# Kernel optimization log

Measured on AMD Instinct MI355X. Metric: run time of the kernel, lower is better.

Reference implementation:

```python
import jax, jax.numpy as jnp
import numpy as np

N, F_IN, F_OUT, P, E = 50000, 64, 64, 8, 800000


def setup_inputs() -> dict:
    key = jax.random.key(0)
    ks = jax.random.split(key, 11)
    s = 0.05
    X = jax.random.normal(ks[0], (N, F_IN, P), jnp.float32)
    edge_index = jax.random.randint(ks[1], (2, E), 0, N)
    edge_weight = jax.random.uniform(ks[2], (E,), jnp.float32)
    # Stacked ChebConv (K=2) params for gates [i, f, c, o]
    Wx0 = jax.random.normal(ks[3], (4, F_IN, F_OUT), jnp.float32) * s
    Wx1 = jax.random.normal(ks[4], (4, F_IN, F_OUT), jnp.float32) * s
    bx = jax.random.normal(ks[5], (4, F_OUT), jnp.float32) * s
    Wh0 = jax.random.normal(ks[6], (4, F_OUT, F_OUT), jnp.float32) * s
    Wh1 = jax.random.normal(ks[7], (4, F_OUT, F_OUT), jnp.float32) * s
    bh = jax.random.normal(ks[8], (4, F_OUT), jnp.float32) * s
    wc = jax.random.normal(ks[9], (3, F_OUT), jnp.float32) * s  # peepholes for i, f, o
    bg = jax.random.normal(ks[10], (4, F_OUT), jnp.float32) * s  # gate biases i, f, c, o
    return dict(X=X, edge_index=edge_index, edge_weight=edge_weight,
                Wx0=Wx0, Wx1=Wx1, bx=bx, Wh0=Wh0, Wh1=Wh1, bh=bh, wc=wc, bg=bg)


def reference(X, edge_index, edge_weight, Wx0, Wx1, bx, Wh0, Wh1, bh, wc, bg):
    src, dst = edge_index[0], edge_index[1]
    # sym-normalized Laplacian, scaled by 2/lambda_max with lambda_max=2, minus I:
    # L_hat = -D^{-1/2} A D^{-1/2}  (diagonal cancels exactly in ChebConv.__norm__)
    deg = jax.ops.segment_sum(edge_weight, src, num_segments=N)
    dis = jnp.where(deg > 0, jax.lax.rsqrt(jnp.maximum(deg, 1e-12)), 0.0)
    wn = -dis[src] * edge_weight * dis[dst]  # [E]

    def cheb(x, W0, W1, b):
        # ChebConv K=2: T0(x)=x, T1(x)=L_hat x ; out = x@W0 + (L_hat x)@W1 + b
        tx1 = jax.ops.segment_sum(wn[:, None] * x[src], dst, num_segments=N)
        return x @ W0 + tx1 @ W1 + b

    def step(Xp):  # one GConvLSTM step from zero hidden/cell state (H=None, C=None)
        H = jnp.zeros((N, F_OUT), X.dtype)
        C = jnp.zeros((N, F_OUT), X.dtype)
        I = jax.nn.sigmoid(cheb(Xp, Wx0[0], Wx1[0], bx[0]) + cheb(H, Wh0[0], Wh1[0], bh[0]) + wc[0] * C + bg[0])
        Fg = jax.nn.sigmoid(cheb(Xp, Wx0[1], Wx1[1], bx[1]) + cheb(H, Wh0[1], Wh1[1], bh[1]) + wc[1] * C + bg[1])
        T = jnp.tanh(cheb(Xp, Wx0[2], Wx1[2], bx[2]) + cheb(H, Wh0[2], Wh1[2], bh[2]) + bg[2])
        Cn = Fg * C + I * T
        O = jax.nn.sigmoid(cheb(Xp, Wx0[3], Wx1[3], bx[3]) + cheb(H, Wh0[3], Wh1[3], bh[3]) + wc[2] * Cn + bg[3])
        return O * jnp.tanh(Cn)

    # periods are independent (fresh zero state each period) -> vmap then sum
    Hs = jax.vmap(step)(jnp.moveaxis(X, 2, 0))  # [P, N, F_OUT]
    return Hs.sum(axis=0)
```

## Files before the change

### kernel.cpp

```cpp
#include <hip/hip_runtime.h>
#include <hip/hip_fp16.h>

#define NN 50000
#define EE 800000
#define FF 64
#define PP 8
#define NPAD 50048
#define ELLW 64

typedef _Float16 half8 __attribute__((ext_vector_type(8)));
typedef _Float16 half4 __attribute__((ext_vector_type(4)));
typedef float floatx4 __attribute__((ext_vector_type(4)));

static constexpr size_t al512(size_t x) { return (x + 511) & ~size_t(511); }
static constexpr size_t OFF_DEG  = 0;
static constexpr size_t OFF_CNT  = al512(OFF_DEG  + (size_t)NN*4);
static constexpr size_t OFF_DIS  = al512(OFF_CNT  + (size_t)NN*4);
static constexpr size_t OFF_ELL  = al512(OFF_DIS  + (size_t)NN*4);
static constexpr size_t OFF_BIAS = al512(OFF_ELL  + (size_t)NN*ELLW*8);
static constexpr size_t OFF_WC2  = al512(OFF_BIAS + 192*4);
static constexpr size_t OFF_WFRG = al512(OFF_WC2  + 64*4);
static constexpr size_t OFF_XB   = al512(OFF_WFRG + (size_t)24576*2);
static constexpr size_t OFF_TB   = al512(OFF_XB   + (size_t)NPAD*512*2);

__global__ void k_build(const int* __restrict__ src, const int* __restrict__ dst,
                        const float* __restrict__ ew,
                        float* __restrict__ deg, int* __restrict__ cnt,
                        int2* __restrict__ ell) {
    int e = blockIdx.x * 256 + threadIdx.x;
    if (e < EE) {
        int s = src[e], d = dst[e];
        float w = ew[e];
        atomicAdd(deg + s, w);
        int pos = atomicAdd(cnt + d, 1);
        if (pos < ELLW) {
            int2 pr; pr.x = s; pr.y = __float_as_int(w);
            ell[(size_t)d * ELLW + pos] = pr;
        }
    }
}

__global__ void k_prep(const float* __restrict__ Wx0, const float* __restrict__ Wx1,
                       const float* __restrict__ bx, const float* __restrict__ bh,
                       const float* __restrict__ wc, const float* __restrict__ bg,
                       const float* __restrict__ deg,
                       _Float16* __restrict__ Wfrag, float* __restrict__ biasv,
                       float* __restrict__ wc2, float* __restrict__ dis) {
    int t = blockIdx.x * 256 + threadIdx.x;
    const int gmap[3] = {0, 2, 3};
    if (t < NN) {
        float dg = deg[t];
        dis[t] = dg > 0.f ? rsqrtf(fmaxf(dg, 1e-12f)) : 0.f;
    }
    if (t < 24576) {
        int j8 = t & 7;
        int lane = (t >> 3) & 63;
        int rem = t >> 9;
        int ct = rem % 12;
        int ks = rem / 12;
        int k = ks * 32 + (lane >> 4) * 8 + j8;
        int gp = ct >> 2;
        int g = gmap[gp];
        int j64 = (ct & 3) * 16 + (lane & 15);
        float val = (k < 64) ? Wx0[((size_t)g * 64 + k) * 64 + j64]
                             : Wx1[((size_t)g * 64 + (k - 64)) * 64 + j64];
        Wfrag[t] = (_Float16)val;
    }
    if (t < 192) {
        int gp = t / 64, j = t % 64;
        int g = gmap[gp];
        biasv[t] = bx[g * 64 + j] + bh[g * 64 + j] + bg[g * 64 + j];
    }
    if (t < 64) wc2[t] = wc[2 * 64 + t];
}

__global__ void k_xw(const float* __restrict__ X, _Float16* __restrict__ XB,
                     const float* __restrict__ dis, const int* __restrict__ cnt,
                     int2* __restrict__ ell) {
    __shared__ _Float16 tile[4][512];
    int wid = threadIdx.x >> 6, lane = threadIdx.x & 63;
    int n = blockIdx.x * 4 + wid;
    if (n >= NN) return;
    int cn = min(cnt[n], ELLW);
    if (lane < cn) {
        int2* p = ell + (size_t)n * ELLW + lane;
        int2 ed = *p;
        float w = dis[ed.x] * __int_as_float(ed.y);
        p->y = __float_as_int(w);
    }
    const float4* xp = (const float4*)(X + (size_t)n * 512 + lane * 8);
    float4 a = xp[0], b = xp[1];
    float v[8] = {a.x, a.y, a.z, a.w, b.x, b.y, b.z, b.w};
#pragma unroll
    for (int p = 0; p < PP; ++p)
        tile[wid][p * 64 + lane] = (_Float16)v[p];
    half8 vv = *(const half8*)&tile[wid][lane * 8];
    *(half8*)(XB + (size_t)n * 512 + lane * 8) = vv;
}

__global__ void k_spmm(const _Float16* __restrict__ XB, const int* __restrict__ cnt,
                       const float* __restrict__ dis, const int2* __restrict__ ell,
                       _Float16* __restrict__ TB, int n_base, int n_end) {
    int wid = threadIdx.x >> 6, lane = threadIdx.x & 63;
    int b = blockIdx.x;
    int half = b & 1;
    int n = n_base + (b >> 1) * 4 + wid;
    if (n >= n_end) return;
    float acc[4] = {0.f, 0.f, 0.f, 0.f};
    int cn = min(cnt[n], ELLW);
    float dn = dis[n];
    const int foff = half * 256 + lane * 4;
    if (cn > 0) {
        const int2* __restrict__ row = ell + (size_t)n * ELLW;
        int2 ed = row[min(lane, cn - 1)];
        int wli = (lane < cn) ? ed.y : 0;
        for (int base = 0; base < cn; base += 16) {
            half4 r[16];
            float wk[16];
#pragma unroll
            for (int u = 0; u < 16; ++u) {
                int srck = __builtin_amdgcn_readlane(ed.x, base + u);
                wk[u] = __int_as_float(__builtin_amdgcn_readlane(wli, base + u));
                r[u] = *(const half4*)(XB + (size_t)srck * 512 + foff);
            }
#pragma unroll
            for (int u = 0; u < 16; ++u) {
#pragma unroll
                for (int j = 0; j < 4; ++j) acc[j] += wk[u] * (float)r[u][j];
            }
        }
    }
    half4 st;
#pragma unroll
    for (int j = 0; j < 4; ++j) st[j] = (_Float16)(-dn * acc[j]);
    *(half4*)(TB + (size_t)n * 512 + foff) = st;
}

__device__ __forceinline__ float fast_rcp(float x) { return __builtin_amdgcn_rcpf(x); }
__device__ __forceinline__ float sigmoidf_fast(float x) {
    return fast_rcp(1.f + __expf(-x));
}
__device__ __forceinline__ float tanhf_fast(float x) {
    return 1.f - 2.f * fast_rcp(1.f + __expf(2.f * x));
}

__global__ __launch_bounds__(64) void k_gemm(const _Float16* __restrict__ XB,
                                             const _Float16* __restrict__ TB,
                                             const _Float16* __restrict__ Wfrag,
                                             const float* __restrict__ biasv,
                                             const float* __restrict__ wc2,
                                             float* __restrict__ out) {
    const int lane = threadIdx.x & 63;
    const half8* __restrict__ Wg8 = (const half8*)Wfrag;

    const int n0 = blockIdx.x * 32;
    const int jj = lane & 15, quad = lane >> 4;

    float bi[4], bc[4], bo[4], wcv[4];
#pragma unroll
    for (int c4 = 0; c4 < 4; ++c4) {
        int j = c4 * 16 + jj;
        bi[c4] = biasv[j];
        bc[c4] = biasv[64 + j];
        bo[c4] = biasv[128 + j];
        wcv[c4] = wc2[j];
    }

    const _Float16* __restrict__ x0 = XB + (size_t)(n0 + jj) * 512;
    const _Float16* __restrict__ x1 = XB + (size_t)(n0 + 16 + jj) * 512;
    const _Float16* __restrict__ t0 = TB + (size_t)(n0 + jj) * 512;
    const _Float16* __restrict__ t1 = TB + (size_t)(n0 + 16 + jj) * 512;

    floatx4 outacc[2][4];
#pragma unroll
    for (int r = 0; r < 2; ++r)
#pragma unroll
        for (int c4 = 0; c4 < 4; ++c4) outacc[r][c4] = (floatx4){0.f, 0.f, 0.f, 0.f};

#pragma unroll 1
    for (int p = 0; p < PP; ++p) {
        const int o = p * 64 + quad * 8;
        half8 a00 = *(const half8*)(x0 + o);
        half8 a01 = *(const half8*)(x0 + o + 32);
        half8 a02 = *(const half8*)(t0 + o);
        half8 a03 = *(const half8*)(t0 + o + 32);
        half8 a10 = *(const half8*)(x1 + o);
        half8 a11 = *(const half8*)(x1 + o + 32);
        half8 a12 = *(const half8*)(t1 + o);
        half8 a13 = *(const half8*)(t1 + o + 32);
#pragma unroll
        for (int c4 = 0; c4 < 4; ++c4) {
            floatx4 ai0 = {0.f,0.f,0.f,0.f}, ac0 = {0.f,0.f,0.f,0.f}, ao0 = {0.f,0.f,0.f,0.f};
            floatx4 ai1 = {0.f,0.f,0.f,0.f}, ac1 = {0.f,0.f,0.f,0.f}, ao1 = {0.f,0.f,0.f,0.f};
#pragma unroll
            for (int ks = 0; ks < 4; ++ks) {
                half8 bfi = Wg8[(ks * 12 + c4) * 64 + lane];
                half8 bfc = Wg8[(ks * 12 + 4 + c4) * 64 + lane];
                half8 bfo = Wg8[(ks * 12 + 8 + c4) * 64 + lane];
                half8 a0 = (ks == 0) ? a00 : (ks == 1) ? a01 : (ks == 2) ? a02 : a03;
                half8 a1 = (ks == 0) ? a10 : (ks == 1) ? a11 : (ks == 2) ? a12 : a13;
                ai0 = __builtin_amdgcn_mfma_f32_16x16x32_f16(a0, bfi, ai0, 0, 0, 0);
                ai1 = __builtin_amdgcn_mfma_f32_16x16x32_f16(a1, bfi, ai1, 0, 0, 0);
                ac0 = __builtin_amdgcn_mfma_f32_16x16x32_f16(a0, bfc, ac0, 0, 0, 0);
                ac1 = __builtin_amdgcn_mfma_f32_16x16x32_f16(a1, bfc, ac1, 0, 0, 0);
                ao0 = __builtin_amdgcn_mfma_f32_16x16x32_f16(a0, bfo, ao0, 0, 0, 0);
                ao1 = __builtin_amdgcn_mfma_f32_16x16x32_f16(a1, bfo, ao1, 0, 0, 0);
            }
#pragma unroll
            for (int rr = 0; rr < 4; ++rr) {
                float I0 = sigmoidf_fast(ai0[rr] + bi[c4]);
                float T0 = tanhf_fast(ac0[rr] + bc[c4]);
                float Cn0 = I0 * T0;
                float O0 = sigmoidf_fast(ao0[rr] + bo[c4] + wcv[c4] * Cn0);
                outacc[0][c4][rr] += O0 * tanhf_fast(Cn0);
                float I1 = sigmoidf_fast(ai1[rr] + bi[c4]);
                float T1 = tanhf_fast(ac1[rr] + bc[c4]);
                float Cn1 = I1 * T1;
                float O1 = sigmoidf_fast(ao1[rr] + bo[c4] + wcv[c4] * Cn1);
                outacc[1][c4][rr] += O1 * tanhf_fast(Cn1);
            }
        }
    }
#pragma unroll
    for (int r = 0; r < 2; ++r)
#pragma unroll
        for (int c4 = 0; c4 < 4; ++c4)
#pragma unroll
            for (int rr = 0; rr < 4; ++rr) {
                int n = n0 + r * 16 + quad * 4 + rr;
                if (n < NN) out[(size_t)n * 64 + c4 * 16 + jj] = outacc[r][c4][rr];
            }
}

extern "C" void kernel_launch(void* const* d_in, const int* in_sizes, int n_in,
                              void* d_out, int out_size, void* d_ws, size_t ws_size,
                              hipStream_t stream) {
    const float* X   = (const float*)d_in[0];
    const int*   ei  = (const int*)d_in[1];
    const float* ew  = (const float*)d_in[2];
    const float* Wx0 = (const float*)d_in[3];
    const float* Wx1 = (const float*)d_in[4];
    const float* bx  = (const float*)d_in[5];
    const float* bh  = (const float*)d_in[8];
    const float* wc  = (const float*)d_in[9];
    const float* bg  = (const float*)d_in[10];
    float* out = (float*)d_out;

    const int* src = ei;
    const int* dst = ei + EE;

    char* ws = (char*)d_ws;
    float* deg     = (float*)(ws + OFF_DEG);
    int*   cnt     = (int*)(ws + OFF_CNT);
    float* dis     = (float*)(ws + OFF_DIS);
    int2*  ell     = (int2*)(ws + OFF_ELL);
    float* biasv   = (float*)(ws + OFF_BIAS);
    float* wc2     = (float*)(ws + OFF_WC2);
    _Float16* Wfrag = (_Float16*)(ws + OFF_WFRG);
    _Float16* XB    = (_Float16*)(ws + OFF_XB);
    _Float16* TB    = (_Float16*)(ws + OFF_TB);

    hipMemsetAsync(ws, 0, OFF_DIS, stream);

    k_build<<<(EE + 255) / 256, 256, 0, stream>>>(src, dst, ew, deg, cnt, ell);
    k_prep<<<196, 256, 0, stream>>>(Wx0, Wx1, bx, bh, wc, bg, deg, Wfrag, biasv, wc2, dis);
    k_xw<<<(NN + 3) / 4, 256, 0, stream>>>(X, XB, dis, cnt, ell);
    for (int r = 0; r < 4; ++r) {
        int nb = r * 12500, ne = min(NN, nb + 12500);
        k_spmm<<<2 * ((ne - nb + 3) / 4), 256, 0, stream>>>(XB, cnt, dis, ell, TB, nb, ne);
    }
    k_gemm<<<NPAD / 32, 64, 0, stream>>>(XB, TB, Wfrag, biasv, wc2, out);
}
```

Baseline: 461.5 us.

## Fuse edge build with X fp16 conversion and fold dis scaling into SpMM

Merges the edge-list/ELL build kernel and the X-to-fp16 transpose into one launch, with separate block ranges for each job, so the two independent memory-bound jobs can overlap. The per-edge dis[src] scaling, previously written back into the ELL by the conversion kernel, is now computed on the fly in the SpMM kernel. The SpMM is also split into two launches instead of four. This removes one kernel launch and one ELL read-modify-write pass, at the cost of an extra gather of dis per edge inside the SpMM.

```diff
diff --git a/kernel.cpp b/kernel.cpp
--- a/kernel.cpp
+++ b/kernel.cpp
@@ -7,6 +7,7 @@
 #define PP 8
 #define NPAD 50048
 #define ELLW 64
+#define NB_BUILD 3125
 
 typedef _Float16 half8 __attribute__((ext_vector_type(8)));
 typedef _Float16 half4 __attribute__((ext_vector_type(4)));
@@ -23,12 +24,15 @@
 static constexpr size_t OFF_XB   = al512(OFF_WFRG + (size_t)24576*2);
 static constexpr size_t OFF_TB   = al512(OFF_XB   + (size_t)NPAD*512*2);
 
-__global__ void k_build(const int* __restrict__ src, const int* __restrict__ dst,
-                        const float* __restrict__ ew,
-                        float* __restrict__ deg, int* __restrict__ cnt,
-                        int2* __restrict__ ell) {
-    int e = blockIdx.x * 256 + threadIdx.x;
-    if (e < EE) {
+__global__ void k_bx(const int* __restrict__ src, const int* __restrict__ dst,
+                     const float* __restrict__ ew,
+                     float* __restrict__ deg, int* __restrict__ cnt,
+                     int2* __restrict__ ell,
+                     const float* __restrict__ X, _Float16* __restrict__ XB) {
+    __shared__ _Float16 tile[4][512];
+    int b = blockIdx.x;
+    if (b < NB_BUILD) {
+        int e = b * 256 + threadIdx.x;
         int s = src[e], d = dst[e];
         float w = ew[e];
         atomicAdd(deg + s, w);
@@ -37,6 +41,17 @@
             int2 pr; pr.x = s; pr.y = __float_as_int(w);
             ell[(size_t)d * ELLW + pos] = pr;
         }
+    } else {
+        int wid = threadIdx.x >> 6, lane = threadIdx.x & 63;
+        int n = (b - NB_BUILD) * 4 + wid;
+        const float4* xp = (const float4*)(X + (size_t)n * 512 + lane * 8);
+        float4 a = xp[0], c = xp[1];
+        float v[8] = {a.x, a.y, a.z, a.w, c.x, c.y, c.z, c.w};
+#pragma unroll
+        for (int p = 0; p < PP; ++p)
+            tile[wid][p * 64 + lane] = (_Float16)v[p];
+        half8 vv = *(const half8*)&tile[wid][lane * 8];
+        *(half8*)(XB + (size_t)n * 512 + lane * 8) = vv;
     }
 }
 
@@ -72,30 +87,6 @@
         biasv[t] = bx[g * 64 + j] + bh[g * 64 + j] + bg[g * 64 + j];
     }
     if (t < 64) wc2[t] = wc[2 * 64 + t];
-}
-
-__global__ void k_xw(const float* __restrict__ X, _Float16* __restrict__ XB,
-                     const float* __restrict__ dis, const int* __restrict__ cnt,
-                     int2* __restrict__ ell) {
-    __shared__ _Float16 tile[4][512];
-    int wid = threadIdx.x >> 6, lane = threadIdx.x & 63;
-    int n = blockIdx.x * 4 + wid;
-    if (n >= NN) return;
-    int cn = min(cnt[n], ELLW);
-    if (lane < cn) {
-        int2* p = ell + (size_t)n * ELLW + lane;
-        int2 ed = *p;
-        float w = dis[ed.x] * __int_as_float(ed.y);
-        p->y = __float_as_int(w);
-    }
-    const float4* xp = (const float4*)(X + (size_t)n * 512 + lane * 8);
-    float4 a = xp[0], b = xp[1];
-    float v[8] = {a.x, a.y, a.z, a.w, b.x, b.y, b.z, b.w};
-#pragma unroll
-    for (int p = 0; p < PP; ++p)
-        tile[wid][p * 64 + lane] = (_Float16)v[p];
-    half8 vv = *(const half8*)&tile[wid][lane * 8];
-    *(half8*)(XB + (size_t)n * 512 + lane * 8) = vv;
 }
 
 __global__ void k_spmm(const _Float16* __restrict__ XB, const int* __restrict__ cnt,
@@ -113,7 +104,8 @@
     if (cn > 0) {
         const int2* __restrict__ row = ell + (size_t)n * ELLW;
         int2 ed = row[min(lane, cn - 1)];
-        int wli = (lane < cn) ? ed.y : 0;
+        float wl = (lane < cn) ? dis[ed.x] * __int_as_float(ed.y) : 0.f;
+        int wli = __float_as_int(wl);
         for (int base = 0; base < cn; base += 16) {
             half4 r[16];
             float wk[16];
@@ -262,11 +254,10 @@
 
     hipMemsetAsync(ws, 0, OFF_DIS, stream);
 
-    k_build<<<(EE + 255) / 256, 256, 0, stream>>>(src, dst, ew, deg, cnt, ell);
+    k_bx<<<NB_BUILD + NN / 4, 256, 0, stream>>>(src, dst, ew, deg, cnt, ell, X, XB);
     k_prep<<<196, 256, 0, stream>>>(Wx0, Wx1, bx, bh, wc, bg, deg, Wfrag, biasv, wc2, dis);
-    k_xw<<<(NN + 3) / 4, 256, 0, stream>>>(X, XB, dis, cnt, ell);
-    for (int r = 0; r < 4; ++r) {
-        int nb = r * 12500, ne = min(NN, nb + 12500);
+    for (int r = 0; r < 2; ++r) {
+        int nb = r * 25000, ne = min(NN, nb + 25000);
         k_spmm<<<2 * ((ne - nb + 3) / 4), 256, 0, stream>>>(XB, cnt, dis, ell, TB, nb, ne);
     }
     k_gemm<<<NPAD / 32, 64, 0, stream>>>(XB, TB, Wfrag, biasv, wc2, out);
```

New measurement: 440.4 us. -4.6%, faster.
